# Kernel tuning notes

Measured on AMD Instinct MI355X. Metric: run time of the kernel, lower is better.

## Reference

```python
import jax, jax.numpy as jnp
import numpy as np
import math

EMBED_DIM = 1024
NUM_HEADS = 16
HEAD_DIM = EMBED_DIM // NUM_HEADS
BATCH = 2
SEQ = 2048


def setup_inputs() -> dict:
    key = jax.random.key(0)
    ks = jax.random.split(key, 9)
    s = 1.0 / math.sqrt(EMBED_DIM)
    return {
        "x": jax.random.normal(ks[0], (BATCH, SEQ, EMBED_DIM), jnp.float32),
        "Wq": jax.random.normal(ks[1], (EMBED_DIM, EMBED_DIM), jnp.float32) * s,
        "bq": jnp.zeros((EMBED_DIM,), jnp.float32),
        "Wk": jax.random.normal(ks[2], (EMBED_DIM, EMBED_DIM), jnp.float32) * s,
        "bk": jnp.zeros((EMBED_DIM,), jnp.float32),
        "Wv": jax.random.normal(ks[3], (EMBED_DIM, EMBED_DIM), jnp.float32) * s,
        "bv": jnp.zeros((EMBED_DIM,), jnp.float32),
        "Wo": jax.random.normal(ks[4], (EMBED_DIM, EMBED_DIM), jnp.float32) * s,
        "bo": jnp.zeros((EMBED_DIM,), jnp.float32),
    }


def _rope_tables(seq_len, dim, dtype):
    inv_freq = 1.0 / (10000.0 ** (jnp.arange(0, dim, 2, dtype=jnp.float32) / dim))
    t = jnp.arange(seq_len, dtype=jnp.float32)
    freqs = jnp.einsum("i,j->ij", t, inv_freq)          # [S, D/2]
    emb = jnp.concatenate([freqs, freqs], axis=-1)       # [S, D]
    return jnp.cos(emb).astype(dtype), jnp.sin(emb).astype(dtype)


def _rotate_half(x):
    x1, x2 = jnp.split(x, 2, axis=-1)
    return jnp.concatenate([-x2, x1], axis=-1)


def _apply_rope(x, cos, sin):
    # x: [B, S, H, D]; cos/sin: [S, D] -> broadcast over batch & heads
    cos = cos[None, :, None, :]
    sin = sin[None, :, None, :]
    return x * cos + _rotate_half(x) * sin


def reference(x, Wq, bq, Wk, bk, Wv, bv, Wo, bo):
    B, S, E = x.shape
    H, D = NUM_HEADS, HEAD_DIM
    q = (x @ Wq + bq).reshape(B, S, H, D)
    k = (x @ Wk + bk).reshape(B, S, H, D)
    v = (x @ Wv + bv).reshape(B, S, H, D)
    cos, sin = _rope_tables(S, D, x.dtype)
    q = _apply_rope(q, cos, sin)
    k = _apply_rope(k, cos, sin)
    scale = 1.0 / math.sqrt(D)
    # scores: [B, H, S, S]
    scores = jnp.einsum("bqhd,bkhd->bhqk", q, k) * scale
    attn = jax.nn.softmax(scores, axis=-1)
    ctx = jnp.einsum("bhqk,bkhd->bqhd", attn, v).reshape(B, S, E)
    return ctx @ Wo + bo
```

## Files before the change

kernel.cpp:

```cpp
#include <hip/hip_runtime.h>
#include <math.h>

#define B_ 2
#define S_ 2048
#define E_ 1024
#define H_ 16
#define D_ 64
#define M_ (B_*S_)

typedef _Float16 f16x8  __attribute__((ext_vector_type(8)));
typedef _Float16 f16x4v __attribute__((ext_vector_type(4)));
typedef __fp16   h16x2  __attribute__((ext_vector_type(2)));
typedef float    f32x4  __attribute__((ext_vector_type(4)));

__device__ __forceinline__ ushort f2h(float f) {
    _Float16 h = (_Float16)f;
    return __builtin_bit_cast(ushort, h);
}

__device__ __forceinline__ void gload_lds16(const ushort* g, ushort* l) {
    __builtin_amdgcn_global_load_lds(
        (const __attribute__((address_space(1))) unsigned int*)g,
        (__attribute__((address_space(3))) unsigned int*)l, 16, 0, 0);
}

__device__ __forceinline__ float exp2_fast(float x) {
    return __builtin_amdgcn_exp2f(x);
}

__global__ void prep_kernel(const float* __restrict__ x,
                            const float* __restrict__ W0, const float* __restrict__ W1,
                            const float* __restrict__ W2, const float* __restrict__ W3,
                            ushort* __restrict__ xf, ushort* __restrict__ WT,
                            float* __restrict__ ct, float* __restrict__ st)
{
    const int bid = blockIdx.x;
    const int tid = threadIdx.x;
    __shared__ float tile[32][33];

    if (bid < 4096) {
        const int z = bid >> 10, rem = bid & 1023;
        const int k0 = (rem >> 5) * 32, nb = (rem & 31) * 32;
        const float* W = (z == 0) ? W0 : (z == 1) ? W1 : (z == 2) ? W2 : W3;
        const size_t zoff = (size_t)z * E_ * E_;
        const int tx = tid & 31, ty = tid >> 5;
        #pragma unroll
        for (int i = 0; i < 4; i++) {
            int r = i * 8 + ty;
            tile[r][tx] = W[(size_t)(k0 + r) * E_ + nb + tx];
        }
        __syncthreads();
        #pragma unroll
        for (int i = 0; i < 4; i++) {
            int r = i * 8 + ty;
            WT[zoff + (size_t)(nb + r) * E_ + k0 + tx] = f2h(tile[tx][r]);
        }
    } else if (bid < 8192) {
        const int i = (bid - 4096) * 1024 + tid * 4;
        float4 v = *(const float4*)&x[i];
        *(ushort4*)&xf[i] = make_ushort4(f2h(v.x), f2h(v.y), f2h(v.z), f2h(v.w));
    } else {
        const int i = (bid - 8192) * 256 + tid;
        const int j = i & 31, pos = i >> 5;
        float invf = (float)pow(10000.0, -(double)j / 32.0);
        float ang  = (float)pos * invf;
        ct[i] = (float)cos((double)ang);
        st[i] = (float)sin((double)ang);
    }
}

#define GBM 128
#define GBN 128
#define GBK 32
#define LOG2E 1.44269504088896340736f

__global__ __launch_bounds__(256, 3)
void gemm_f16(const ushort* __restrict__ A, const ushort* __restrict__ WTp,
              const float* __restrict__ b0, const float* __restrict__ b1,
              const float* __restrict__ b2,
              const float* __restrict__ ct, const float* __restrict__ st,
              ushort* __restrict__ outQ, ushort* __restrict__ outK,
              ushort* __restrict__ outV, float* __restrict__ outF,
              int force_mode)
{
    __shared__ __align__(16) ushort lA[3][GBM * GBK];
    __shared__ __align__(16) ushort lB[3][GBN * GBK];

    const int tid  = threadIdx.x;
    const int wv   = tid >> 6, lane = tid & 63;
    const int c    = lane & 15, qd = lane >> 4;
    const int rh   = wv >> 1, chn = wv & 1;

    const int mode = (force_mode >= 0) ? force_mode : (int)blockIdx.z;
    const size_t zoff = (force_mode >= 0) ? 0 : (size_t)blockIdx.z * (E_ * E_);
    const ushort* Bt = WTp + zoff;

    const int m0 = (blockIdx.x & 31) * GBM;
    const int n0 = (blockIdx.x >> 5) * GBN;

    const ushort* gsrc = (wv < 2) ? A : Bt;
    const int rowbase = ((wv < 2) ? m0 : n0) + (wv & 1) * 64;
    const int lofs = (wv & 1) * 64 * GBK;
    const int srow = lane >> 2;
    const int soct = (lane & 3) * 8;

    f32x4 acc[4][4] = {};

    #pragma unroll
    for (int pt = 0; pt < 2; pt++) {
        ushort* dst = ((wv < 2) ? &lA[pt][0] : &lB[pt][0]) + lofs;
        const int k0i = pt * GBK;
        #pragma unroll
        for (int cc = 0; cc < 4; cc++) {
            const ushort* g = gsrc + (size_t)(rowbase + cc * 16 + srow) * E_ + k0i + soct;
            gload_lds16(g, dst + cc * 512);
        }
    }
    __builtin_amdgcn_s_waitcnt(0x0F74);
    __builtin_amdgcn_s_barrier();

    for (int t = 0; t < E_ / GBK; t++) {
        if (t + 2 < E_ / GBK) {
            const int bi = (t + 2) % 3;
            const int k0i = (t + 2) * GBK;
            ushort* dst = ((wv < 2) ? &lA[bi][0] : &lB[bi][0]) + lofs;
            #pragma unroll
            for (int cc = 0; cc < 4; cc++) {
                const ushort* g = gsrc + (size_t)(rowbase + cc * 16 + srow) * E_ + k0i + soct;
                gload_lds16(g, dst + cc * 512);
            }
        }

        const ushort* Ab = lA[t % 3];
        const ushort* Bb = lB[t % 3];

        f16x8 af[4], bf[4];
        #pragma unroll
        for (int mt = 0; mt < 4; mt++)
            af[mt] = *(const f16x8*)&Ab[(rh * 64 + mt * 16 + c) * GBK + qd * 8];
        #pragma unroll
        for (int nt = 0; nt < 4; nt++)
            bf[nt] = *(const f16x8*)&Bb[(chn * 64 + nt * 16 + c) * GBK + qd * 8];
        #pragma unroll
        for (int mt = 0; mt < 4; mt++)
            #pragma unroll
            for (int nt = 0; nt < 4; nt++)
                acc[mt][nt] = __builtin_amdgcn_mfma_f32_16x16x32_f16(af[mt], bf[nt], acc[mt][nt], 0, 0, 0);

        if (t < E_ / GBK - 2) {
            __builtin_amdgcn_s_waitcnt(0x0F74);
            __builtin_amdgcn_s_barrier();
        } else if (t == E_ / GBK - 2) {
            __builtin_amdgcn_s_waitcnt(0x0F70);
            __builtin_amdgcn_s_barrier();
        }
    }

    const float* bias = (mode == 0) ? b0 : (mode == 1) ? b1 : (mode == 2) ? b2 : b0;
    const int colbase = n0 + chn * 64;

    if (mode == 3) {
        #pragma unroll
        for (int mt = 0; mt < 4; mt++)
            #pragma unroll
            for (int r = 0; r < 4; r++) {
                const int row = m0 + rh * 64 + mt * 16 + qd * 4 + r;
                #pragma unroll
                for (int nt = 0; nt < 4; nt++) {
                    const int col = colbase + nt * 16 + c;
                    outF[(size_t)row * E_ + col] = acc[mt][nt][r] + bias[col];
                }
            }
    } else if (mode == 2) {
        const int hd = colbase >> 6;
        const int xr = c & 3;
        #pragma unroll
        for (int mt = 0; mt < 4; mt++)
            #pragma unroll
            for (int r = 0; r < 4; r++) {
                const int row = m0 + rh * 64 + mt * 16 + qd * 4 + r;
                const int bb = row >> 11, sl = row & (S_ - 1);
                const int g  = sl >> 5, k32 = sl & 31;
                const int q2 = (k32 >> 2) & 3, kh = k32 >> 4, kj = k32 & 3;
                const size_t base = (size_t)(bb * H_ + hd) * (S_ * D_)
                                  + g * 2048 + ((q2 ^ xr) << 3) + kh * 4 + kj;
                #pragma unroll
                for (int nt = 0; nt < 4; nt++) {
                    const int d = nt * 16 + c;
                    outV[base + (size_t)d * 32] = f2h(acc[mt][nt][r] + bias[colbase + d]);
                }
            }
    } else {
        ushort* O = (mode == 0) ? outQ : outK;
        const float sc = (mode == 0) ? 0.125f * LOG2E : 1.0f;
        #pragma unroll
        for (int mt = 0; mt < 4; mt++)
            #pragma unroll
            for (int r = 0; r < 4; r++) {
                const int row = m0 + rh * 64 + mt * 16 + qd * 4 + r;
                const int pos = row & (S_ - 1);
                const int sw = row & 7;
                #pragma unroll
                for (int p = 0; p < 2; p++) {
                    const int j32 = p * 16 + c;
                    const float cth = ct[pos * 32 + j32], sth = st[pos * 32 + j32];
                    const float v1 = acc[mt][p][r]     + bias[colbase + p * 16 + c];
                    const float v2 = acc[mt][p + 2][r] + bias[colbase + (p + 2) * 16 + c];
                    const float o1 = (v1 * cth - v2 * sth) * sc;
                    const float o2 = (v2 * cth + v1 * sth) * sc;
                    const int cd1 = p * 16 + c, cd2 = cd1 + 32;
                    O[(size_t)row * E_ + colbase + (((cd1 >> 3) ^ sw) * 8) + (cd1 & 7)] = f2h(o1);
                    O[(size_t)row * E_ + colbase + (((cd2 >> 3) ^ sw) * 8) + (cd2 & 7)] = f2h(o2);
                }
            }
    }
}

__global__ __launch_bounds__(256, 3)
void attn_mfma(const ushort* __restrict__ Qf, const ushort* __restrict__ Kf,
               const ushort* __restrict__ Vfg, ushort* __restrict__ ctxf)
{
    __shared__ __align__(16) ushort L[24576];

    const int tid = threadIdx.x;
    const int wv = tid >> 6, lane = tid & 63;
    const int c = lane & 15, qd = lane >> 4;
    const int cs = c & 7;

    const int xcd = blockIdx.x & 7, ii = blockIdx.x >> 3;
    const int bh = xcd * 4 + (ii & 3);
    const int qtb = ii >> 2;
    const int b = bh >> 4, h = bh & 15;
    const int q0 = qtb * 64;

    const size_t qrow0 = (size_t)b * S_ + q0;
    const size_t krow0 = (size_t)b * S_;
    const size_t vbase = (size_t)bh * (S_ * D_);

    const int l8 = lane >> 3, l7 = lane & 7;

    #pragma unroll
    for (int j = 0; j < 2; j++) {
        const int row = wv * 16 + j * 8 + l8;
        gload_lds16(Qf + (qrow0 + row) * E_ + h * 64 + l7 * 8, &L[wv * 1024 + j * 512]);
    }
    __syncthreads();
    f16x8 qfrag[4][2];
    #pragma unroll
    for (int qt = 0; qt < 4; qt++)
        #pragma unroll
        for (int kc = 0; kc < 2; kc++)
            qfrag[qt][kc] = *(const f16x8*)&L[(qt * 16 + c) * 64 + (((kc * 4 + qd) ^ cs) * 8)];
    __syncthreads();

    f32x4 acc[4][4] = {};
    float lsum[4] = {0.f, 0.f, 0.f, 0.f};

    ushort* const myL = &L[wv * 6144];
    const int vxo = (qd ^ (c & 3)) << 3;

    #pragma unroll
    for (int j = 0; j < 2; j++)
        gload_lds16(Kf + (krow0 + wv * 32 + j * 8 + l8) * E_ + h * 64 + l7 * 8,
                    myL + j * 512);
    #pragma unroll
    for (int j = 0; j < 2; j++)
        gload_lds16(Vfg + vbase + (size_t)wv * 2048 + j * 512 + lane * 8,
                    myL + 2048 + j * 512);

    #pragma unroll 1
    for (int T = 0; T < 16; T++) {
        uint4 bfu[4];

        {
            const int g1 = T * 4 + wv;
            ushort* vdst = myL + 2048 + (T & 1) * 2048 + 1024;
            #pragma unroll
            for (int j = 0; j < 2; j++)
                gload_lds16(Kf + (krow0 + g1 * 32 + 16 + j * 8 + l8) * E_ + h * 64 + l7 * 8,
                            myL + 1024 + j * 512);
            #pragma unroll
            for (int j = 0; j < 2; j++)
                gload_lds16(Vfg + vbase + (size_t)g1 * 2048 + 1024 + j * 512 + lane * 8,
                            vdst + j * 512);
            __builtin_amdgcn_s_waitcnt(0x0F74);

            const ushort* kb = myL;
            f16x8 kf0 = *(const f16x8*)&kb[c * 64 + ((qd ^ cs) * 8)];
            f16x8 kf1 = *(const f16x8*)&kb[c * 64 + (((4 + qd) ^ cs) * 8)];
            #pragma unroll
            for (int qt = 0; qt < 4; qt++) {
                f32x4 s = {};
                s = __builtin_amdgcn_mfma_f32_16x16x32_f16(kf0, qfrag[qt][0], s, 0, 0, 0);
                s = __builtin_amdgcn_mfma_f32_16x16x32_f16(kf1, qfrag[qt][1], s, 0, 0, 0);
                const float p0 = exp2_fast(s[0]), p1 = exp2_fast(s[1]);
                const float p2 = exp2_fast(s[2]), p3 = exp2_fast(s[3]);
                lsum[qt] += (p0 + p1) + (p2 + p3);
                bfu[qt].x = __builtin_bit_cast(unsigned int, __builtin_amdgcn_cvt_pkrtz(p0, p1));
                bfu[qt].y = __builtin_bit_cast(unsigned int, __builtin_amdgcn_cvt_pkrtz(p2, p3));
            }
        }

        {
            if (T < 15) {
                const int g2 = (T + 1) * 4 + wv;
                ushort* vdst = myL + 2048 + ((T + 1) & 1) * 2048;
                #pragma unroll
                for (int j = 0; j < 2; j++)
                    gload_lds16(Kf + (krow0 + g2 * 32 + j * 8 + l8) * E_ + h * 64 + l7 * 8,
                                myL + j * 512);
                #pragma unroll
                for (int j = 0; j < 2; j++)
                    gload_lds16(Vfg + vbase + (size_t)g2 * 2048 + j * 512 + lane * 8,
                                vdst + j * 512);
                __builtin_amdgcn_s_waitcnt(0x0F74);
            } else {
                __builtin_amdgcn_s_waitcnt(0x0F70);
            }

            const ushort* kb = myL + 1024;
            f16x8 kf0 = *(const f16x8*)&kb[c * 64 + ((qd ^ cs) * 8)];
            f16x8 kf1 = *(const f16x8*)&kb[c * 64 + (((4 + qd) ^ cs) * 8)];
            #pragma unroll
            for (int qt = 0; qt < 4; qt++) {
                f32x4 s = {};
                s = __builtin_amdgcn_mfma_f32_16x16x32_f16(kf0, qfrag[qt][0], s, 0, 0, 0);
                s = __builtin_amdgcn_mfma_f32_16x16x32_f16(kf1, qfrag[qt][1], s, 0, 0, 0);
                const float p0 = exp2_fast(s[0]), p1 = exp2_fast(s[1]);
                const float p2 = exp2_fast(s[2]), p3 = exp2_fast(s[3]);
                lsum[qt] += (p0 + p1) + (p2 + p3);
                bfu[qt].z = __builtin_bit_cast(unsigned int, __builtin_amdgcn_cvt_pkrtz(p0, p1));
                bfu[qt].w = __builtin_bit_cast(unsigned int, __builtin_amdgcn_cvt_pkrtz(p2, p3));
            }
        }

        const ushort* vb = myL + 2048 + (T & 1) * 2048;
        __builtin_amdgcn_s_setprio(1);
        #pragma unroll
        for (int dt = 0; dt < 4; dt++) {
            f16x8 vfr = *(const f16x8*)&vb[(dt * 16 + c) * 32 + vxo];
            #pragma unroll
            for (int qt = 0; qt < 4; qt++)
                acc[dt][qt] = __builtin_amdgcn_mfma_f32_16x16x32_f16(
                    vfr, __builtin_bit_cast(f16x8, bfu[qt]), acc[dt][qt], 0, 0, 0);
        }
        __builtin_amdgcn_s_setprio(0);
    }

    __syncthreads();

    float* red = (float*)&L[0];
    float* lsr = (float*)&L[8192];

    #pragma unroll
    for (int qt = 0; qt < 4; qt++) {
        float v = lsum[qt];
        v += __shfl_xor(v, 16);
        v += __shfl_xor(v, 32);
        lsum[qt] = v;
    }
    if (lane < 16) {
        #pragma unroll
        for (int qt = 0; qt < 4; qt++) lsr[wv * 64 + qt * 16 + lane] = lsum[qt];
    }

    f32x4 own[4];
    #pragma unroll
    for (int qt = 0; qt < 4; qt++)
        own[qt] = (wv == 0) ? acc[0][qt] : (wv == 1) ? acc[1][qt]
                : (wv == 2) ? acc[2][qt] : acc[3][qt];

    #pragma unroll
    for (int r = 1; r < 4; r++) {
        const int ds = (wv + r) & 3;
        #pragma unroll
        for (int qt = 0; qt < 4; qt++) {
            f32x4 sv = (ds == 0) ? acc[0][qt] : (ds == 1) ? acc[1][qt]
                     : (ds == 2) ? acc[2][qt] : acc[3][qt];
            *(f32x4*)&red[ds * 1024 + qt * 256 + lane * 4] = sv;
        }
        __syncthreads();
        #pragma unroll
        for (int qt = 0; qt < 4; qt++)
            own[qt] += *(const f32x4*)&red[wv * 1024 + qt * 256 + lane * 4];
        if (r < 3) __syncthreads();
    }

    float inv[4];
    #pragma unroll
    for (int qt = 0; qt < 4; qt++) {
        const int q = qt * 16 + c;
        inv[qt] = 1.0f / (lsr[q] + lsr[64 + q] + lsr[128 + q] + lsr[192 + q]);
    }

    const size_t obase = qrow0 * E_ + h * 64 + wv * 16 + qd * 4;
    #pragma unroll
    for (int qt = 0; qt < 4; qt++) {
        f32x4 v = own[qt];
        const float iq = inv[qt];
        ushort4 o = make_ushort4(f2h(v[0] * iq), f2h(v[1] * iq),
                                 f2h(v[2] * iq), f2h(v[3] * iq));
        *(ushort4*)&ctxf[obase + (size_t)(qt * 16 + c) * E_] = o;
    }
}

extern "C" void kernel_launch(void* const* d_in, const int* in_sizes, int n_in,
                              void* d_out, int out_size, void* d_ws, size_t ws_size,
                              hipStream_t stream)
{
    const float* x  = (const float*)d_in[0];
    const float* Wq = (const float*)d_in[1];
    const float* bq = (const float*)d_in[2];
    const float* Wk = (const float*)d_in[3];
    const float* bk = (const float*)d_in[4];
    const float* Wv = (const float*)d_in[5];
    const float* bv = (const float*)d_in[6];
    const float* Wo = (const float*)d_in[7];
    const float* bo = (const float*)d_in[8];
    float* out = (float*)d_out;

    ushort* Qb = (ushort*)d_ws;
    ushort* Kb = Qb + (size_t)M_ * E_;
    ushort* Vf = Kb + (size_t)M_ * E_;
    ushort* xf = Vf + (size_t)M_ * E_;
    ushort* WT = xf + (size_t)M_ * E_;
    float*  ct = (float*)(WT + (size_t)4 * E_ * E_);
    float*  st = ct + S_ * 32;
    ushort* ctxf = Qb;

    hipLaunchKernelGGL(prep_kernel, dim3(8448), dim3(256), 0, stream,
                       x, Wq, Wk, Wv, Wo, xf, WT, ct, st);

    hipLaunchKernelGGL(gemm_f16, dim3(256, 1, 3), dim3(256), 0, stream,
                       xf, WT, bq, bk, bv, ct, st,
                       Qb, Kb, Vf, (float*)nullptr, -1);

    hipLaunchKernelGGL(attn_mfma, dim3(B_ * H_ * (S_ / 64)), dim3(256), 0, stream,
                       Qb, Kb, Vf, ctxf);

    hipLaunchKernelGGL(gemm_f16, dim3(256), dim3(256), 0, stream,
                       ctxf, WT + (size_t)3 * E_ * E_, bo, bo, bo, ct, st,
                       (ushort*)nullptr, (ushort*)nullptr, (ushort*)nullptr, out, 3);
}
```

Measured before the change: 179.4 us.

## Strength-reduce attention load addresses, batch QK MFMAs, and change V swizzle

The attention loop now keeps running pointers for the K and V tile loads and advances them, instead of recomputing 64-bit addresses on every iteration. The QK^T MFMAs for all four query tiles are issued back to back at raised priority before any exp2, which should give the matrix unit a denser burst and let the exponentials overlap. The V XOR swizzle key changes from c&3 to (c>>2)&3 in both the V-projection writer and the reader, which changes the LDS bank-conflict pattern. Holding four score vectors at once raises register pressure.

```diff
diff --git a/kernel.cpp b/kernel.cpp
--- a/kernel.cpp
+++ b/kernel.cpp
@@ -173,7 +173,7 @@
             }
     } else if (mode == 2) {
         const int hd = colbase >> 6;
-        const int xr = c & 3;
+        const int xr = (c >> 2) & 3;
         #pragma unroll
         for (int mt = 0; mt < 4; mt++)
             #pragma unroll
@@ -257,44 +257,48 @@
     float lsum[4] = {0.f, 0.f, 0.f, 0.f};
 
     ushort* const myL = &L[wv * 6144];
-    const int vxo = (qd ^ (c & 3)) << 3;
-
-    #pragma unroll
-    for (int j = 0; j < 2; j++)
-        gload_lds16(Kf + (krow0 + wv * 32 + j * 8 + l8) * E_ + h * 64 + l7 * 8,
-                    myL + j * 512);
-    #pragma unroll
-    for (int j = 0; j < 2; j++)
-        gload_lds16(Vfg + vbase + (size_t)wv * 2048 + j * 512 + lane * 8,
-                    myL + 2048 + j * 512);
+    const int vxo = (qd ^ ((c >> 2) & 3)) << 3;
+
+    const ushort* kst0 = Kf + (krow0 + wv * 32 + l8) * E_ + h * 64 + l7 * 8;
+    const ushort* kst1 = kst0 + 8 * E_;
+    const ushort* vstA = Vfg + vbase + (size_t)wv * 2048 + lane * 8;
+    const ushort* vstB = vstA + 512;
+
+    gload_lds16(kst0, myL);
+    gload_lds16(kst1, myL + 512);
+    gload_lds16(vstA, myL + 2048);
+    gload_lds16(vstB, myL + 2560);
+    kst0 += 16 * E_; kst1 += 16 * E_; vstA += 1024; vstB += 1024;
 
     #pragma unroll 1
     for (int T = 0; T < 16; T++) {
         uint4 bfu[4];
 
         {
-            const int g1 = T * 4 + wv;
-            ushort* vdst = myL + 2048 + (T & 1) * 2048 + 1024;
-            #pragma unroll
-            for (int j = 0; j < 2; j++)
-                gload_lds16(Kf + (krow0 + g1 * 32 + 16 + j * 8 + l8) * E_ + h * 64 + l7 * 8,
-                            myL + 1024 + j * 512);
-            #pragma unroll
-            for (int j = 0; j < 2; j++)
-                gload_lds16(Vfg + vbase + (size_t)g1 * 2048 + 1024 + j * 512 + lane * 8,
-                            vdst + j * 512);
+            ushort* vd = myL + 2048 + (T & 1) * 2048 + 1024;
+            gload_lds16(kst0, myL + 1024);
+            gload_lds16(kst1, myL + 1536);
+            gload_lds16(vstA, vd);
+            gload_lds16(vstB, vd + 512);
+            kst0 += 112 * E_; kst1 += 112 * E_; vstA += 7168; vstB += 7168;
             __builtin_amdgcn_s_waitcnt(0x0F74);
 
             const ushort* kb = myL;
             f16x8 kf0 = *(const f16x8*)&kb[c * 64 + ((qd ^ cs) * 8)];
             f16x8 kf1 = *(const f16x8*)&kb[c * 64 + (((4 + qd) ^ cs) * 8)];
+            f32x4 sv[4];
+            __builtin_amdgcn_s_setprio(1);
             #pragma unroll
             for (int qt = 0; qt < 4; qt++) {
                 f32x4 s = {};
                 s = __builtin_amdgcn_mfma_f32_16x16x32_f16(kf0, qfrag[qt][0], s, 0, 0, 0);
-                s = __builtin_amdgcn_mfma_f32_16x16x32_f16(kf1, qfrag[qt][1], s, 0, 0, 0);
-                const float p0 = exp2_fast(s[0]), p1 = exp2_fast(s[1]);
-                const float p2 = exp2_fast(s[2]), p3 = exp2_fast(s[3]);
+                sv[qt] = __builtin_amdgcn_mfma_f32_16x16x32_f16(kf1, qfrag[qt][1], s, 0, 0, 0);
+            }
+            __builtin_amdgcn_s_setprio(0);
+            #pragma unroll
+            for (int qt = 0; qt < 4; qt++) {
+                const float p0 = exp2_fast(sv[qt][0]), p1 = exp2_fast(sv[qt][1]);
+                const float p2 = exp2_fast(sv[qt][2]), p3 = exp2_fast(sv[qt][3]);
                 lsum[qt] += (p0 + p1) + (p2 + p3);
                 bfu[qt].x = __builtin_bit_cast(unsigned int, __builtin_amdgcn_cvt_pkrtz(p0, p1));
                 bfu[qt].y = __builtin_bit_cast(unsigned int, __builtin_amdgcn_cvt_pkrtz(p2, p3));
@@ -303,16 +307,12 @@
 
         {
             if (T < 15) {
-                const int g2 = (T + 1) * 4 + wv;
-                ushort* vdst = myL + 2048 + ((T + 1) & 1) * 2048;
-                #pragma unroll
-                for (int j = 0; j < 2; j++)
-                    gload_lds16(Kf + (krow0 + g2 * 32 + j * 8 + l8) * E_ + h * 64 + l7 * 8,
-                                myL + j * 512);
-                #pragma unroll
-                for (int j = 0; j < 2; j++)
-                    gload_lds16(Vfg + vbase + (size_t)g2 * 2048 + j * 512 + lane * 8,
-                                vdst + j * 512);
+                ushort* vd = myL + 2048 + ((T + 1) & 1) * 2048;
+                gload_lds16(kst0, myL);
+                gload_lds16(kst1, myL + 512);
+                gload_lds16(vstA, vd);
+                gload_lds16(vstB, vd + 512);
+                kst0 += 16 * E_; kst1 += 16 * E_; vstA += 1024; vstB += 1024;
                 __builtin_amdgcn_s_waitcnt(0x0F74);
             } else {
                 __builtin_amdgcn_s_waitcnt(0x0F70);
@@ -321,13 +321,19 @@
             const ushort* kb = myL + 1024;
             f16x8 kf0 = *(const f16x8*)&kb[c * 64 + ((qd ^ cs) * 8)];
             f16x8 kf1 = *(const f16x8*)&kb[c * 64 + (((4 + qd) ^ cs) * 8)];
+            f32x4 sv[4];
+            __builtin_amdgcn_s_setprio(1);
             #pragma unroll
             for (int qt = 0; qt < 4; qt++) {
                 f32x4 s = {};
                 s = __builtin_amdgcn_mfma_f32_16x16x32_f16(kf0, qfrag[qt][0], s, 0, 0, 0);
-                s = __builtin_amdgcn_mfma_f32_16x16x32_f16(kf1, qfrag[qt][1], s, 0, 0, 0);
-                const float p0 = exp2_fast(s[0]), p1 = exp2_fast(s[1]);
-                const float p2 = exp2_fast(s[2]), p3 = exp2_fast(s[3]);
+                sv[qt] = __builtin_amdgcn_mfma_f32_16x16x32_f16(kf1, qfrag[qt][1], s, 0, 0, 0);
+            }
+            __builtin_amdgcn_s_setprio(0);
+            #pragma unroll
+            for (int qt = 0; qt < 4; qt++) {
+                const float p0 = exp2_fast(sv[qt][0]), p1 = exp2_fast(sv[qt][1]);
+                const float p2 = exp2_fast(sv[qt][2]), p3 = exp2_fast(sv[qt][3]);
                 lsum[qt] += (p0 + p1) + (p2 + p3);
                 bfu[qt].z = __builtin_bit_cast(unsigned int, __builtin_amdgcn_cvt_pkrtz(p0, p1));
                 bfu[qt].w = __builtin_bit_cast(unsigned int, __builtin_amdgcn_cvt_pkrtz(p2, p3));
```

After: 182.4 us. No clear change (+1.7%).
